# Kernel optimization log

Hardware: AMD Instinct MI355X
Metric: run time of the kernel (lower is better)

The kernel has to match this reference:

```python
import jax, jax.numpy as jnp
import numpy as np


def setup_inputs() -> dict:
    key = jax.random.key(0)
    ks = jax.random.split(key, 7)
    B, T, E, H, V = 32, 200, 32, 128, 8000
    s = lambda fan: 1.0 / np.sqrt(fan)
    return {
        "x": jax.random.normal(ks[0], (B, T, E), dtype=jnp.float32),
        "Ww": jax.random.normal(ks[1], (H, H), dtype=jnp.float32) * s(H),
        "Wb": jax.random.normal(ks[2], (H,), dtype=jnp.float32) * s(H),
        "Uw": jax.random.normal(ks[3], (H, E), dtype=jnp.float32) * s(E),
        "Ub": jax.random.normal(ks[4], (H,), dtype=jnp.float32) * s(E),
        "Vw": jax.random.normal(ks[5], (V, H), dtype=jnp.float32) * s(H),
        "Vb": jax.random.normal(ks[6], (V,), dtype=jnp.float32) * s(H),
    }


def reference(x, Ww, Wb, Uw, Ub, Vw, Vb):
    # x: [B, T, E]. Elman RNN: h_t = tanh(W h_{t-1} + b_W + U x_t + b_U); out_t = V h_t + b_V
    B = x.shape[0]
    H = Ww.shape[0]
    h0 = jnp.zeros((B, H), dtype=x.dtype)
    # Precompute input projections for all timesteps at once: [T, B, H]
    ux = jnp.einsum('bte,he->tbh', x, Uw) + Ub + Wb

    def step(h, ux_t):
        h = jnp.tanh(h @ Ww.T + ux_t)
        return h, h

    hidden, hs = jax.lax.scan(step, h0, ux)  # hs: [T, B, H]
    # Output projection applied to all hidden states (same math as per-step V)
    out_seq = jnp.einsum('tbh,vh->btv', hs, Vw) + Vb  # [B, T, V]
    return out_seq, hidden
```

## Files before the change

### kernel.cpp

```cpp
#include <hip/hip_runtime.h>
#include <stdint.h>

typedef short v8s __attribute__((ext_vector_type(8)));
typedef float v4f __attribute__((ext_vector_type(4)));

__device__ __forceinline__ float bf2f(short s) {
    unsigned int u = ((unsigned int)(unsigned short)s) << 16;
    float f; __builtin_memcpy(&f, &u, 4); return f;
}
__device__ __forceinline__ unsigned short f2bf_rne(float f) {
    unsigned int u; __builtin_memcpy(&u, &f, 4);
    return (unsigned short)((u + 0x7FFFu + ((u >> 16) & 1u)) >> 16);
}
__device__ __forceinline__ unsigned short f2bf_rhu(float f) {
    unsigned int u; __builtin_memcpy(&u, &f, 4);
    return (unsigned short)((u + 0x8000u) >> 16);
}
__device__ __forceinline__ unsigned short f2bf_trunc(float f) {
    unsigned int u; __builtin_memcpy(&u, &f, 4);
    return (unsigned short)(u >> 16);
}
__device__ __forceinline__ float tanh_fast(float z) {
    float e = __expf(2.0f * z);
    float r = __builtin_amdgcn_rcpf(e + 1.0f);
    return __builtin_fmaf(-2.0f, r, 1.0f);
}

__global__ __launch_bounds__(256) void ux_kernel(
    const float* __restrict__ x, const float* __restrict__ Uw,
    const float* __restrict__ Ub, const float* __restrict__ Wb,
    float* __restrict__ ux) {
    int row = blockIdx.x * 2 + (threadIdx.x >> 7);
    int i = threadIdx.x & 127;
    int b = row & 31, t = row >> 5;
    const float* xr = x + (b * 200 + t) * 32;
    const float* ur = Uw + i * 32;
    float acc = 0.f;
#pragma unroll
    for (int e4 = 0; e4 < 8; ++e4) {
        v4f xv = *(const v4f*)(xr + e4 * 4);
        v4f uv = *(const v4f*)(ur + e4 * 4);
#pragma unroll
        for (int j = 0; j < 4; ++j) acc = __builtin_fmaf(xv[j], uv[j], acc);
    }
    ux[row * 128 + i] = acc + Ub[i] + Wb[i];
}

__global__ __launch_bounds__(256) void vwcvt_kernel(
    const float* __restrict__ Vw, short* __restrict__ vwb) {
    int i = (blockIdx.x * 256 + threadIdx.x) * 8;
    v4f p0 = *(const v4f*)(Vw + i);
    v4f p1 = *(const v4f*)(Vw + i + 4);
    v8s o;
#pragma unroll
    for (int j = 0; j < 4; ++j) {
        o[j] = (short)f2bf_rne(p0[j]);
        o[4 + j] = (short)f2bf_rne(p1[j]);
    }
    *(v8s*)(vwb + i) = o;
}

__global__ __launch_bounds__(512) void rnn_kernel(
    const float* __restrict__ Ww, const float* __restrict__ ux,
    short* __restrict__ hs, float* __restrict__ hidden_out) {
    __shared__ alignas(16) short hbuf[2 * 2 * 16 * 136];
    char* lds = (char*)hbuf;
    const int tid = threadIdx.x;
    const int w = tid >> 6, lane = tid & 63, q = lane >> 4, c = lane & 15;
    const int b0 = blockIdx.x * 16;
    const int col = 16 * w + c;

    for (int i = tid; i < 1088; i += 512) ((v8s*)hbuf)[i] = (v8s){0, 0, 0, 0, 0, 0, 0, 0};

    v8s w_hi[4], w_lo[4];
#pragma unroll
    for (int kb = 0; kb < 4; ++kb) {
        const float* p = Ww + col * 128 + 32 * kb + 8 * q;
#pragma unroll
        for (int j = 0; j < 8; ++j) {
            float v = p[j];
            unsigned short hi = f2bf_rne(v);
            w_hi[kb][j] = (short)hi;
            w_lo[kb][j] = (short)f2bf_rne(v - bf2f((short)hi));
        }
    }

    const int rd_base = c * 272 + 16 * q;
    const int wr_base = q * 1088 + col * 2;

    const float* uxp = ux + (b0 + 4 * q) * 128 + col;
    float uxv0 = uxp[0], uxv1 = uxp[128], uxv2 = uxp[256], uxv3 = uxp[384];
    uxp += 4096;
    short* hsp = hs + (b0 + 4 * q) * 128 + col;

    __syncthreads();

#define RNN_STEP(RBUF, WBUF)                                                        \
    {                                                                               \
        float un0 = uxp[0], un1 = uxp[128], un2 = uxp[256], un3 = uxp[384];         \
        v4f a0 = {uxv0, uxv1, uxv2, uxv3};                                          \
        v4f a1 = {0.f, 0.f, 0.f, 0.f}, a2 = a1;                                     \
        _Pragma("unroll") for (int kb = 0; kb < 4; ++kb) {                          \
            v8s ahi = *(const v8s*)(lds + (RBUF)*8704 + kb * 64 + rd_base);         \
            v8s alo = *(const v8s*)(lds + (RBUF)*8704 + 4352 + kb * 64 + rd_base);  \
            a0 = __builtin_amdgcn_mfma_f32_16x16x32_bf16(ahi, w_hi[kb], a0, 0, 0, 0); \
            a1 = __builtin_amdgcn_mfma_f32_16x16x32_bf16(ahi, w_lo[kb], a1, 0, 0, 0); \
            a2 = __builtin_amdgcn_mfma_f32_16x16x32_bf16(alo, w_hi[kb], a2, 0, 0, 0); \
        }                                                                           \
        _Pragma("unroll") for (int r = 0; r < 4; ++r) {                             \
            float z = (a0[r] + a1[r]) + a2[r];                                      \
            float h = tanh_fast(z);                                                 \
            unsigned short hh = f2bf_rhu(h);                                        \
            float rem = h - bf2f((short)hh);                                        \
            unsigned short hl = f2bf_trunc(rem);                                    \
            *(short*)(lds + (WBUF)*8704 + r * 272 + wr_base) = (short)hh;           \
            *(short*)(lds + (WBUF)*8704 + 4352 + r * 272 + wr_base) = (short)hl;    \
            hsp[r * 128] = (short)hh;                                               \
        }                                                                           \
        uxv0 = un0; uxv1 = un1; uxv2 = un2; uxv3 = un3;                             \
        uxp += 4096; hsp += 4096;                                                   \
        __syncthreads();                                                            \
    }

    for (int tp = 0; tp < 100; ++tp) {
        RNN_STEP(0, 1)
        RNN_STEP(1, 0)
    }
#undef RNN_STEP

#pragma unroll
    for (int r = 0; r < 4; ++r) {
        short hh = *(short*)(lds + r * 272 + wr_base);
        short hl = *(short*)(lds + 4352 + r * 272 + wr_base);
        hidden_out[(b0 + 4 * q + r) * 128 + col] = bf2f(hh) + bf2f(hl);
    }
}

__global__ __launch_bounds__(256) void out_kernel(
    const short* __restrict__ hs, const short* __restrict__ vwb,
    const float* __restrict__ Vb, float* __restrict__ out) {
    const int tid = threadIdx.x;
    const int w = tid >> 6, lane = tid & 63, q = lane >> 4, c = lane & 15;
    const int v_wave = blockIdx.x * 128 + 32 * w;
    const int n0 = blockIdx.y * 128;

    v4f acc[2][8];
#pragma unroll
    for (int a = 0; a < 2; ++a)
#pragma unroll
        for (int b = 0; b < 8; ++b) acc[a][b] = (v4f){0.f, 0.f, 0.f, 0.f};

#pragma unroll
    for (int kb = 0; kb < 4; ++kb) {
        v8s afr[2];
#pragma unroll
        for (int vt = 0; vt < 2; ++vt) {
            int vr = v_wave + 16 * vt + c;
            vr = vr < 8000 ? vr : 7999;
            afr[vt] = *(const v8s*)(vwb + vr * 128 + 32 * kb + 8 * q);
        }
#pragma unroll
        for (int nt = 0; nt < 8; ++nt) {
            v8s bfr = *(const v8s*)(hs + (n0 + 16 * nt + c) * 128 + 32 * kb + 8 * q);
            acc[0][nt] = __builtin_amdgcn_mfma_f32_16x16x32_bf16(afr[0], bfr, acc[0][nt], 0, 0, 0);
            acc[1][nt] = __builtin_amdgcn_mfma_f32_16x16x32_bf16(afr[1], bfr, acc[1][nt], 0, 0, 0);
        }
    }

#pragma unroll
    for (int vt = 0; vt < 2; ++vt) {
        int v4base = v_wave + 16 * vt + 4 * q;
        bool ok = v4base < 8000;
        v4f vbv = *(const v4f*)(Vb + (ok ? v4base : 0));
#pragma unroll
        for (int nt = 0; nt < 8; ++nt) {
            int n = n0 + 16 * nt + c;
            int t = n >> 5, b = n & 31;
            unsigned int off = (unsigned int)(b * 200 + t) * 8000u + (unsigned int)v4base;
            if (ok) {
                v4f o;
#pragma unroll
                for (int r = 0; r < 4; ++r) o[r] = acc[vt][nt][r] + vbv[r];
                *(v4f*)(out + (size_t)off) = o;
            }
        }
    }
}

extern "C" void kernel_launch(void* const* d_in, const int* in_sizes, int n_in,
                              void* d_out, int out_size, void* d_ws, size_t ws_size,
                              hipStream_t stream) {
    const float* x  = (const float*)d_in[0];
    const float* Ww = (const float*)d_in[1];
    const float* Wb = (const float*)d_in[2];
    const float* Uw = (const float*)d_in[3];
    const float* Ub = (const float*)d_in[4];
    const float* Vw = (const float*)d_in[5];
    const float* Vb = (const float*)d_in[6];
    float* out = (float*)d_out;

    float* ux = (float*)d_ws;
    short* hs = (short*)((char*)d_ws + 3276800);
    short* vwb = (short*)d_ws;

    ux_kernel<<<3200, 256, 0, stream>>>(x, Uw, Ub, Wb, ux);
    rnn_kernel<<<2, 512, 0, stream>>>(Ww, ux, hs, out + 51200000);
    vwcvt_kernel<<<500, 256, 0, stream>>>(Vw, vwb);
    dim3 g(63, 50);
    out_kernel<<<g, 256, 0, stream>>>(hs, vwb, Vb, out);
}
```

Baseline: 405.0 us.

## Fuse RNN recurrence and output projection with ticketed producer-consumer overlap

Merges the recurrent kernel and the output GEMM into one persistent-style launch. Blocks take an atomic ticket: the first two run the recurrence and publish a per-tile release flag every four timesteps, and the rest spin on their tile's flag before computing the vocab projection. This lets the large output GEMM overlap the long serial recurrence instead of running after it. The separate Vw-to-bf16 conversion kernel is removed and the conversion is done inline when fragments are loaded. The cost is redundant Vw conversion per block, spin-wait overhead, and reliance on the ticket order so the producer blocks are always scheduled.

```diff
diff --git a/kernel.cpp b/kernel.cpp
--- a/kernel.cpp
+++ b/kernel.cpp
@@ -29,7 +29,10 @@
 __global__ __launch_bounds__(256) void ux_kernel(
     const float* __restrict__ x, const float* __restrict__ Uw,
     const float* __restrict__ Ub, const float* __restrict__ Wb,
-    float* __restrict__ ux) {
+    float* __restrict__ ux, unsigned* __restrict__ sync) {
+    if (blockIdx.x == 0) {
+        for (int i = threadIdx.x; i < 864; i += 256) sync[i] = 0;
+    }
     int row = blockIdx.x * 2 + (threadIdx.x >> 7);
     int i = threadIdx.x & 127;
     int b = row & 31, t = row >> 5;
@@ -46,54 +49,53 @@
     ux[row * 128 + i] = acc + Ub[i] + Wb[i];
 }
 
-__global__ __launch_bounds__(256) void vwcvt_kernel(
-    const float* __restrict__ Vw, short* __restrict__ vwb) {
-    int i = (blockIdx.x * 256 + threadIdx.x) * 8;
-    v4f p0 = *(const v4f*)(Vw + i);
-    v4f p1 = *(const v4f*)(Vw + i + 4);
-    v8s o;
-#pragma unroll
-    for (int j = 0; j < 4; ++j) {
-        o[j] = (short)f2bf_rne(p0[j]);
-        o[4 + j] = (short)f2bf_rne(p1[j]);
-    }
-    *(v8s*)(vwb + i) = o;
-}
-
-__global__ __launch_bounds__(512) void rnn_kernel(
+__global__ __launch_bounds__(512) void fused_kernel(
     const float* __restrict__ Ww, const float* __restrict__ ux,
-    short* __restrict__ hs, float* __restrict__ hidden_out) {
+    short* __restrict__ hs, float* __restrict__ hidden_out,
+    const float* __restrict__ Vw, const float* __restrict__ Vb,
+    float* __restrict__ out, unsigned* __restrict__ sync) {
     __shared__ alignas(16) short hbuf[2 * 2 * 16 * 136];
-    char* lds = (char*)hbuf;
+    __shared__ unsigned s_ticket;
     const int tid = threadIdx.x;
+
+    if (tid == 0)
+        s_ticket = __hip_atomic_fetch_add(sync, 1u, __ATOMIC_RELAXED,
+                                          __HIP_MEMORY_SCOPE_AGENT);
+    __syncthreads();
+    const unsigned ticket = s_ticket;
+
     const int w = tid >> 6, lane = tid & 63, q = lane >> 4, c = lane & 15;
-    const int b0 = blockIdx.x * 16;
-    const int col = 16 * w + c;
-
-    for (int i = tid; i < 1088; i += 512) ((v8s*)hbuf)[i] = (v8s){0, 0, 0, 0, 0, 0, 0, 0};
-
-    v8s w_hi[4], w_lo[4];
-#pragma unroll
-    for (int kb = 0; kb < 4; ++kb) {
-        const float* p = Ww + col * 128 + 32 * kb + 8 * q;
-#pragma unroll
-        for (int j = 0; j < 8; ++j) {
-            float v = p[j];
-            unsigned short hi = f2bf_rne(v);
-            w_hi[kb][j] = (short)hi;
-            w_lo[kb][j] = (short)f2bf_rne(v - bf2f((short)hi));
-        }
-    }
-
-    const int rd_base = c * 272 + 16 * q;
-    const int wr_base = q * 1088 + col * 2;
-
-    const float* uxp = ux + (b0 + 4 * q) * 128 + col;
-    float uxv0 = uxp[0], uxv1 = uxp[128], uxv2 = uxp[256], uxv3 = uxp[384];
-    uxp += 4096;
-    short* hsp = hs + (b0 + 4 * q) * 128 + col;
-
-    __syncthreads();
+
+    if (ticket < 2) {
+        char* lds = (char*)hbuf;
+        const int b0 = (int)ticket * 16;
+        const int col = 16 * w + c;
+
+        for (int i = tid; i < 1088; i += 512)
+            ((v8s*)hbuf)[i] = (v8s){0, 0, 0, 0, 0, 0, 0, 0};
+
+        v8s w_hi[4], w_lo[4];
+#pragma unroll
+        for (int kb = 0; kb < 4; ++kb) {
+            const float* p = Ww + col * 128 + 32 * kb + 8 * q;
+#pragma unroll
+            for (int j = 0; j < 8; ++j) {
+                float v = p[j];
+                unsigned short hi = f2bf_rne(v);
+                w_hi[kb][j] = (short)hi;
+                w_lo[kb][j] = (short)f2bf_rne(v - bf2f((short)hi));
+            }
+        }
+
+        const int rd_base = c * 272 + 16 * q;
+        const int wr_base = q * 1088 + col * 2;
+
+        const float* uxp = ux + (b0 + 4 * q) * 128 + col;
+        float uxv0 = uxp[0], uxv1 = uxp[128], uxv2 = uxp[256], uxv3 = uxp[384];
+        uxp += 4096;
+        short* hsp = hs + (b0 + 4 * q) * 128 + col;
+
+        __syncthreads();
 
 #define RNN_STEP(RBUF, WBUF)                                                        \
     {                                                                               \
@@ -122,27 +124,40 @@
         __syncthreads();                                                            \
     }
 
-    for (int tp = 0; tp < 100; ++tp) {
-        RNN_STEP(0, 1)
-        RNN_STEP(1, 0)
-    }
+        for (int tp = 0; tp < 100; ++tp) {
+            RNN_STEP(0, 1)
+            RNN_STEP(1, 0)
+            if ((tp & 1) && tid == 0)
+                __hip_atomic_fetch_add(sync + 16 + (tp >> 1) * 16, 1u,
+                                       __ATOMIC_RELEASE, __HIP_MEMORY_SCOPE_AGENT);
+        }
 #undef RNN_STEP
 
 #pragma unroll
-    for (int r = 0; r < 4; ++r) {
-        short hh = *(short*)(lds + r * 272 + wr_base);
-        short hl = *(short*)(lds + 4352 + r * 272 + wr_base);
-        hidden_out[(b0 + 4 * q + r) * 128 + col] = bf2f(hh) + bf2f(hl);
-    }
-}
-
-__global__ __launch_bounds__(256) void out_kernel(
-    const short* __restrict__ hs, const short* __restrict__ vwb,
-    const float* __restrict__ Vb, float* __restrict__ out) {
-    const int tid = threadIdx.x;
-    const int w = tid >> 6, lane = tid & 63, q = lane >> 4, c = lane & 15;
-    const int v_wave = blockIdx.x * 128 + 32 * w;
-    const int n0 = blockIdx.y * 128;
+        for (int r = 0; r < 4; ++r) {
+            short hh = *(short*)(lds + r * 272 + wr_base);
+            short hl = *(short*)(lds + 4352 + r * 272 + wr_base);
+            hidden_out[(b0 + 4 * q + r) * 128 + col] = bf2f(hh) + bf2f(hl);
+        }
+        return;
+    }
+
+    const int cid = (int)ticket - 2;
+    const int tb_tile = cid >> 5;
+    const int v_tile = cid & 31;
+    const int v_wave = v_tile * 256 + 32 * w;
+    const int n0 = tb_tile * 128;
+
+    unsigned* flag = sync + 16 + tb_tile * 16;
+    if (tid == 0) {
+        while (__hip_atomic_load(flag, __ATOMIC_RELAXED,
+                                 __HIP_MEMORY_SCOPE_AGENT) < 2u)
+            __builtin_amdgcn_s_sleep(32);
+        unsigned g = __hip_atomic_load(flag, __ATOMIC_ACQUIRE,
+                                       __HIP_MEMORY_SCOPE_AGENT);
+        asm volatile("" ::"v"(g));
+    }
+    __syncthreads();
 
     v4f acc[2][8];
 #pragma unroll
@@ -157,7 +172,14 @@
         for (int vt = 0; vt < 2; ++vt) {
             int vr = v_wave + 16 * vt + c;
             vr = vr < 8000 ? vr : 7999;
-            afr[vt] = *(const v8s*)(vwb + vr * 128 + 32 * kb + 8 * q);
+            const float* ap = Vw + vr * 128 + 32 * kb + 8 * q;
+            v4f p0 = *(const v4f*)ap;
+            v4f p1 = *(const v4f*)(ap + 4);
+#pragma unroll
+            for (int j = 0; j < 4; ++j) {
+                afr[vt][j] = (short)f2bf_rne(p0[j]);
+                afr[vt][4 + j] = (short)f2bf_rne(p1[j]);
+            }
         }
 #pragma unroll
         for (int nt = 0; nt < 8; ++nt) {
@@ -201,11 +223,9 @@
 
     float* ux = (float*)d_ws;
     short* hs = (short*)((char*)d_ws + 3276800);
-    short* vwb = (short*)d_ws;
-
-    ux_kernel<<<3200, 256, 0, stream>>>(x, Uw, Ub, Wb, ux);
-    rnn_kernel<<<2, 512, 0, stream>>>(Ww, ux, hs, out + 51200000);
-    vwcvt_kernel<<<500, 256, 0, stream>>>(Vw, vwb);
-    dim3 g(63, 50);
-    out_kernel<<<g, 256, 0, stream>>>(hs, vwb, Vb, out);
-}
+    unsigned* sync = (unsigned*)((char*)d_ws + 4915200);
+
+    ux_kernel<<<3200, 256, 0, stream>>>(x, Uw, Ub, Wb, ux, sync);
+    fused_kernel<<<1602, 512, 0, stream>>>(Ww, ux, hs, out + 51200000,
+                                           Vw, Vb, out, sync);
+}
```

Measured after the change: 388.2 us. 1.04x faster.
